# Kernel optimization log

Measured on AMD Instinct MI355X. Metric: run time of the kernel, lower is better.

## Reference

```python
import jax, jax.numpy as jnp
import numpy as np

# static config (mirrors params)
T, B, NA, NF = 48, 256, 23, 4
D = NA * NF          # y_dim = 92
XD = 2               # x_dim
H = 128              # rnn_dim
HD = 128             # h_dim
NL = 2               # n_layers
FS = 0.1
BURN = 12
IN_ENC = XD + D + H  # GRU input size = 222
A0, A1 = 12, 11      # agents 0..11 -> net0, 12..22 -> net1


def setup_inputs() -> dict:
    key = jax.random.key(0)
    ks = jax.random.split(key, 16)
    s = 0.05
    rn = lambda k, shape: jax.random.normal(k, shape, jnp.float32) * s
    return {
        "states": jax.random.normal(ks[0], (T + 1, 1, B, D), jnp.float32),
        # per-network (leading dim 2) GRU layer-0 and layer-1 weights (torch GRU layout: [r|z|n])
        "W_ih0": rn(ks[1], (2, 3 * H, IN_ENC)),
        "W_hh0": rn(ks[2], (2, 3 * H, H)),
        "b_ih0": rn(ks[3], (2, 3 * H)),
        "b_hh0": rn(ks[4], (2, 3 * H)),
        "W_ih1": rn(ks[5], (2, 3 * H, H)),
        "W_hh1": rn(ks[6], (2, 3 * H, H)),
        "b_ih1": rn(ks[7], (2, 3 * H)),
        "b_hh1": rn(ks[8], (2, 3 * H)),
        # decoder MLP (dropout is identity in eval) + mean head
        "W1": rn(ks[9], (2, HD, H)),
        "b1": rn(ks[10], (2, HD)),
        "W2": rn(ks[11], (2, HD, HD)),
        "b2": rn(ks[12], (2, HD)),
        "Wm": rn(ks[13], (2, XD, HD)),
        "bm": rn(ks[14], (2, XD)),
        "rollout": 0,
        "train": 0,
    }


def _gru_cell(x, h, Wih, Whh, bih, bhh):
    gi = x @ Wih.T + bih
    gh = h @ Whh.T + bhh
    r = jax.nn.sigmoid(gi[:, :H] + gh[:, :H])
    z = jax.nn.sigmoid(gi[:, H:2 * H] + gh[:, H:2 * H])
    n = jnp.tanh(gi[:, 2 * H:] + r * gh[:, 2 * H:])
    return (1.0 - z) * n + z * h


def _batch_error(a, b):
    # sum over batch of the euclidean norm over features
    return jnp.sum(jnp.sqrt(jnp.sum((a - b) ** 2, axis=1)))


def _group_step(h, y_t, y3, y3n, lo, hi, g, P):
    # h: [NL, A*B, H]; agents lo..hi-1 of network g, folded into the batch dim
    A = hi - lo
    vel = y3[:, lo:hi, 2:4].transpose(1, 0, 2).reshape(A * B, 2)
    pos = y3[:, lo:hi, 0:2].transpose(1, 0, 2).reshape(A * B, 2)
    vel_true = y3n[:, lo:hi, 2:4].transpose(1, 0, 2).reshape(A * B, 2)
    pos_true = y3n[:, lo:hi, 0:2].transpose(1, 0, 2).reshape(A * B, 2)
    y_rep = jnp.broadcast_to(y_t[None], (A, B, D)).reshape(A * B, D)
    h_last = h[-1]
    enc_in = jnp.concatenate([vel, y_rep, h_last], axis=1)  # [A*B, IN_ENC]
    # decoder uses the PRE-update hidden state
    d = jax.nn.relu(h_last @ P["W1"][g].T + P["b1"][g])
    d = jax.nn.relu(d @ P["W2"][g].T + P["b2"][g])
    dm = d @ P["Wm"][g].T + P["bm"][g]  # [A*B, XD]
    # 2-layer GRU step
    h0n = _gru_cell(enc_in, h[0], P["W_ih0"][g], P["W_hh0"][g], P["b_ih0"][g], P["b_hh0"][g])
    h1n = _gru_cell(h0n, h[1], P["W_ih1"][g], P["W_hh1"][g], P["b_ih1"][g], P["b_hh1"][g])
    h_new = jnp.stack([h0n, h1n])
    L = _batch_error(dm, vel_true)
    ep = _batch_error(pos + vel * FS, pos_true)
    ev = _batch_error(dm[:, :2], vel_true)
    return h_new, L, ep, ev


def _forward(states, P):
    y_seq = states[:T, 0]       # [T, B, D]
    y_next = states[1:T + 1, 0]  # [T, B, D]

    def step(carry, xs):
        h0, h1, L, ep, ev = carry
        y_t, y_t1, t = xs
        y3 = y_t.reshape(B, NA, NF)
        y3n = y_t1.reshape(B, NA, NF)
        h0n, L0, ep0, ev0 = _group_step(h0, y_t, y3, y3n, 0, A0, 0, P)
        h1n, L1, ep1, ev1 = _group_step(h1, y_t, y3, y3n, A0, NA, 1, P)
        m = (t >= BURN).astype(jnp.float32)
        return (h0n, h1n, L + L0 + L1, ep + m * (ep0 + ep1), ev + m * (ev0 + ev1)), None

    init = (jnp.zeros((NL, A0 * B, H), jnp.float32),
            jnp.zeros((NL, A1 * B, H), jnp.float32),
            jnp.zeros((), jnp.float32), jnp.zeros((), jnp.float32), jnp.zeros((), jnp.float32))
    (h0, h1, L, ep, ev), _ = jax.lax.scan(step, init, (y_seq, y_next, jnp.arange(T)))
    L_rec = L / (T * NA)
    e_pos = ep / ((T - BURN) * NA)
    e_vel = ev / ((T - BURN) * NA)
    return L_rec, e_pos, e_vel


def reference(states, W_ih0, W_hh0, b_ih0, b_hh0, W_ih1, W_hh1, b_ih1, b_hh1,
              W1, b1, W2, b2, Wm, bm, rollout, train):
    P = dict(W_ih0=W_ih0, W_hh0=W_hh0, b_ih0=b_ih0, b_hh0=b_hh0,
             W_ih1=W_ih1, W_hh1=W_hh1, b_ih1=b_ih1, b_hh1=b_hh1,
             W1=W1, b1=b1, W2=W2, b2=b2, Wm=Wm, bm=bm)
    return _forward(states, P)
```

## Files before the change

kernel.cpp:

```cpp
#include <hip/hip_runtime.h>
#include <hip/hip_bf16.h>


typedef unsigned short u16;
typedef unsigned int u32;
typedef unsigned char u8;
typedef long i64;
typedef __attribute__((ext_vector_type(4))) float f32x4;

#define MFMA_F8(acc, a, b) (acc) = __builtin_amdgcn_mfma_f32_16x16x32_fp8_fp8((i64)(a), (i64)(b), (acc), 0, 0, 0)

__device__ __forceinline__ void pin(i64& x) { asm volatile("" : "+v"(x)); }

__device__ __forceinline__ u8 f2e4(float v) {
  return (u8)(__builtin_amdgcn_cvt_pk_fp8_f32(v, 0.f, 0, false) & 0xff);
}
__device__ __forceinline__ u32 pk4(float a, float b, float c, float d) {
  u32 p = (u32)__builtin_amdgcn_cvt_pk_fp8_f32(a, b, 0, false);
  return (u32)__builtin_amdgcn_cvt_pk_fp8_f32(c, d, (int)p, true);
}
__device__ __forceinline__ float sigf(float x) {
  return __builtin_amdgcn_rcpf(1.f + __expf(-x));
}
__device__ __forceinline__ float tanh_fast(float x) {
  return 1.f - 2.f * __builtin_amdgcn_rcpf(1.f + __expf(2.f * x));
}

constexpr int E0 = 2 * 384 * 352;
constexpr int E1 = E0 + 2 * 384 * 256;
constexpr int E2 = E1 + 2 * 128 * 128;
constexpr int E3 = E2 + 2 * 128 * 128;
constexpr int E4 = E3 + 2 * 128 * 128;
constexpr int E5 = E4 + 2 * 128 * 128;
constexpr int NBIAS = 2048;
constexpr int TOTAL = E5 + NBIAS + 4;
constexpr int WB_BYTE_OFF = 16384;

__global__ void prep_kernel(const float* __restrict__ Wih0, const float* __restrict__ Whh0,
                            const float* __restrict__ bih0, const float* __restrict__ bhh0,
                            const float* __restrict__ Wih1, const float* __restrict__ Whh1,
                            const float* __restrict__ bih1, const float* __restrict__ bhh1,
                            const float* __restrict__ W1, const float* __restrict__ W2,
                            u8* __restrict__ wb, float* __restrict__ wsf) {
  for (int idx = blockIdx.x * blockDim.x + threadIdx.x; idx < TOTAL;
       idx += gridDim.x * blockDim.x) {
    if (idx < E0) {
      int g = idx / 135168;
      int r = idx - g * 135168;
      int j = r / 352;
      int k = r - j * 352;
      const float* wi = Wih0 + (g * 384 + j) * 222;
      float v;
      if (k < 94) v = wi[k];
      else if (k < 96) v = 0.f;
      else if (k < 224) v = wi[k - 2];
      else v = Whh0[(g * 384 + j) * 128 + (k - 224)];
      wb[idx] = f2e4(v);
    } else if (idx < E1) {
      int q = idx - E0;
      int g = q / 98304;
      int r = q - g * 98304;
      int j = r >> 8;
      int k = r & 255;
      float v = (k < 128) ? Wih1[(g * 384 + j) * 128 + k]
                          : Whh1[(g * 384 + j) * 128 + (k - 128)];
      wb[idx] = f2e4(v);
    } else if (idx < E2) {
      int q = idx - E1; int g = q >> 14; int r = q & 16383; int j = r >> 7; int k = r & 127;
      wb[idx] = f2e4(Whh0[(g * 384 + 256 + j) * 128 + k]);
    } else if (idx < E3) {
      int q = idx - E2; int g = q >> 14; int r = q & 16383; int j = r >> 7; int k = r & 127;
      wb[idx] = f2e4(Whh1[(g * 384 + 256 + j) * 128 + k]);
    } else if (idx < E4) {
      int q = idx - E3; int g = q >> 14; int r = q & 16383; int j = r >> 7; int k = r & 127;
      wb[idx] = f2e4(W1[(g * 128 + j) * 128 + k]);
    } else if (idx < E5) {
      int q = idx - E4; int g = q >> 14; int r = q & 16383; int j = r >> 7; int k = r & 127;
      wb[idx] = f2e4(W2[(g * 128 + j) * 128 + k]);
    } else if (idx < E5 + NBIAS) {
      int q = idx - E5;
      float v;
      if (q < 512)       { int g = q >> 8, j = q & 255;              v = bih0[g*384 + j] + bhh0[g*384 + j]; }
      else if (q < 768)  { int p = q - 512;  int g = p >> 7, j = p & 127; v = bih0[g*384 + 256 + j]; }
      else if (q < 1024) { int p = q - 768;  int g = p >> 7, j = p & 127; v = bhh0[g*384 + 256 + j]; }
      else if (q < 1536) { int p = q - 1024; int g = p >> 8, j = p & 255; v = bih1[g*384 + j] + bhh1[g*384 + j]; }
      else if (q < 1792) { int p = q - 1536; int g = p >> 7, j = p & 127; v = bih1[g*384 + 256 + j]; }
      else               { int p = q - 1792; int g = p >> 7, j = p & 127; v = bhh1[g*384 + 256 + j]; }
      wsf[4 + q] = v;
    } else {
      wsf[idx - (E5 + NBIAS)] = 0.f;
    }
  }
}

__global__ __launch_bounds__(512, 2) __attribute__((amdgpu_waves_per_eu(2, 2)))
void rnn_kernel(const float* __restrict__ states,
                const u8* __restrict__ wb,
                float* __restrict__ wsf,
                const float* __restrict__ b1g,
                const float* __restrict__ b2g,
                const float* __restrict__ Wmg,
                const float* __restrict__ bmg) {
  const int blk = blockIdx.x;
  const int g = (blk < 96) ? 0 : 1;
  const int r0 = (g == 0) ? (blk * 32) : ((blk - 96) * 32);
  const int aAg = (g == 0 ? 0 : 12) + (r0 >> 8);
  const int b0 = r0 & 255;

  const int tid = threadIdx.x;
  const int wid = tid >> 6;
  const int ln = tid & 63;
  const int j_in = ln & 15;
  const int kq = ln >> 4;
  const int c0 = wid * 16 + kq * 4;

  __shared__ __align__(16) u8 h0b[2][32 * 136];
  __shared__ __align__(16) u8 h1b[2][32 * 136];
  __shared__ __align__(16) u8 yb[2][32 * 104];
  __shared__ __align__(16) u8 d1b[32 * 136];
  __shared__ __align__(16) u8 d2b[32 * 136];
  __shared__ __align__(16) float bias[1536];
  __shared__ float dmv[48][32][2];
  __shared__ float red[8][3];

  const u8* W0   = wb + g * 135168;
  const u8* W1c  = wb + E0 + g * 98304;
  const u8* Wn0p = wb + E1 + g * 16384;
  const u8* Wn1p = wb + E2 + g * 16384;
  const u8* Wm1p = wb + E3 + g * 16384;
  const u8* Wm2p = wb + E4 + g * 16384;
  const int jh = wid * 16 + j_in;

  i64 w0r[11], w0z[11], w0n[7];
#pragma unroll
  for (int kt = 0; kt < 11; ++kt) {
    w0r[kt] = *(const i64*)(W0 + (jh)       * 352 + kt * 32 + kq * 8);
    w0z[kt] = *(const i64*)(W0 + (128 + jh) * 352 + kt * 32 + kq * 8);
    if (kt < 7) w0n[kt] = *(const i64*)(W0 + (256 + jh) * 352 + kt * 32 + kq * 8);
  }
  i64 w1r[8], w1z[8], w1n[4];
#pragma unroll
  for (int kt = 0; kt < 8; ++kt) {
    w1r[kt] = *(const i64*)(W1c + (jh)       * 256 + kt * 32 + kq * 8);
    w1z[kt] = *(const i64*)(W1c + (128 + jh) * 256 + kt * 32 + kq * 8);
    if (kt < 4) w1n[kt] = *(const i64*)(W1c + (256 + jh) * 256 + kt * 32 + kq * 8);
  }
  i64 wn0[4], wn1[4], wm1[4], wm2[4];
#pragma unroll
  for (int kt = 0; kt < 4; ++kt) {
    wn0[kt] = *(const i64*)(Wn0p + jh * 128 + kt * 32 + kq * 8);
    wn1[kt] = *(const i64*)(Wn1p + jh * 128 + kt * 32 + kq * 8);
    wm1[kt] = *(const i64*)(Wm1p + jh * 128 + kt * 32 + kq * 8);
    wm2[kt] = *(const i64*)(Wm2p + jh * 128 + kt * 32 + kq * 8);
  }
#pragma unroll
  for (int kt = 0; kt < 11; ++kt) { pin(w0r[kt]); pin(w0z[kt]); }
#pragma unroll
  for (int kt = 0; kt < 7; ++kt) pin(w0n[kt]);
#pragma unroll
  for (int kt = 0; kt < 8; ++kt) { pin(w1r[kt]); pin(w1z[kt]); }
#pragma unroll
  for (int kt = 0; kt < 4; ++kt) {
    pin(w1n[kt]); pin(wn0[kt]); pin(wn1[kt]); pin(wm1[kt]); pin(wm2[kt]);
  }

  for (int i = tid; i < 1536; i += 512) {
    float v;
    if (i < 256)       v = wsf[4 + g * 256 + i];
    else if (i < 384)  v = wsf[516 + g * 128 + (i - 256)];
    else if (i < 512)  v = wsf[772 + g * 128 + (i - 384)];
    else if (i < 768)  v = wsf[1028 + g * 256 + (i - 512)];
    else if (i < 896)  v = wsf[1540 + g * 128 + (i - 768)];
    else if (i < 1024) v = wsf[1796 + g * 128 + (i - 896)];
    else if (i < 1152) v = b1g[g * 128 + (i - 1024)];
    else if (i < 1280) v = b2g[g * 128 + (i - 1152)];
    else               v = Wmg[g * 256 + (i - 1280)];
    bias[i] = v;
  }
  for (int i = tid; i < 32 * 136; i += 512) { h0b[0][i] = 0; h1b[0][i] = 0; }
  for (int idx = tid; idx < 768; idx += 512) {
    int i = idx / 24, k4 = idx - i * 24;
    const float* srow = states + ((size_t)(b0 + i)) * 92;
    float v0, v1, v2, v3;
    if (k4 == 0) { v0 = srow[aAg*4+2]; v1 = srow[aAg*4+3]; v2 = srow[0]; v3 = srow[1]; }
    else {
      int kk = k4 * 4 - 2;
      v0 = srow[kk]; v1 = srow[kk+1];
      v2 = (kk+2 < 92) ? srow[kk+2] : 0.f;
      v3 = (kk+3 < 92) ? srow[kk+3] : 0.f;
    }
    *(u32*)(&yb[0][i * 104 + k4 * 4]) = pk4(v0, v1, v2, v3);
  }

  f32x4 hv0[2] = {{0,0,0,0},{0,0,0,0}};
  f32x4 hv1[2] = {{0,0,0,0},{0,0,0,0}};
  __syncthreads();

  for (int t = 0; t < 48; ++t) {
    const int cur = t & 1, nxt = cur ^ 1;
    const u8* h0c = h0b[cur]; u8* h0n = h0b[nxt];
    const u8* h1c = h1b[cur]; u8* h1n = h1b[nxt];
    const u8* ybc = yb[cur];  u8* ybn = yb[nxt];

    float yst[2][4];
#pragma unroll
    for (int q = 0; q < 2; ++q) {
      int idx = tid + q * 512;
      if (idx < 768) {
        int i = idx / 24, k4 = idx - i * 24;
        const float* srow = states + ((size_t)((t + 1) * 256 + b0 + i)) * 92;
        if (k4 == 0) { yst[q][0]=srow[aAg*4+2]; yst[q][1]=srow[aAg*4+3]; yst[q][2]=srow[0]; yst[q][3]=srow[1]; }
        else {
          int kk = k4 * 4 - 2;
          yst[q][0] = srow[kk]; yst[q][1] = srow[kk+1];
          yst[q][2] = (kk+2 < 92) ? srow[kk+2] : 0.f;
          yst[q][3] = (kk+3 < 92) ? srow[kk+3] : 0.f;
        }
      }
    }

    const u8* pH1a = h1c + j_in * 136 + kq * 8;
    const u8* pH1b = h1c + (16 + j_in) * 136 + kq * 8;
    const u8* pH0a = h0c + j_in * 136 + kq * 8;
    const u8* pH0b = h0c + (16 + j_in) * 136 + kq * 8;
    const u8* pYa  = ybc + j_in * 104 + kq * 8;
    const u8* pYb  = ybc + (16 + j_in) * 104 + kq * 8;

    {
      f32x4 m0 = {0,0,0,0}, m1 = {0,0,0,0};
#pragma unroll
      for (int kt = 0; kt < 4; ++kt) {
        i64 bb0 = *(const i64*)(pH1a + kt * 32);
        i64 bb1 = *(const i64*)(pH1b + kt * 32);
        MFMA_F8(m0, wm1[kt], bb0);
        MFMA_F8(m1, wm1[kt], bb1);
      }
      f32x4 b1v = *(const f32x4*)(bias + 1024 + c0);
      *(u32*)(d1b + j_in * 136 + c0) =
        pk4(fmaxf(m0[0]+b1v[0],0.f), fmaxf(m0[1]+b1v[1],0.f), fmaxf(m0[2]+b1v[2],0.f), fmaxf(m0[3]+b1v[3],0.f));
      *(u32*)(d1b + (16 + j_in) * 136 + c0) =
        pk4(fmaxf(m1[0]+b1v[0],0.f), fmaxf(m1[1]+b1v[1],0.f), fmaxf(m1[2]+b1v[2],0.f), fmaxf(m1[3]+b1v[3],0.f));
    }

    {
      f32x4 aR[2] = {{0,0,0,0},{0,0,0,0}};
      f32x4 aZ[2] = {{0,0,0,0},{0,0,0,0}};
      f32x4 aN[2] = {{0,0,0,0},{0,0,0,0}};
      f32x4 aG[2] = {{0,0,0,0},{0,0,0,0}};
#pragma unroll
      for (int kt = 0; kt < 11; ++kt) {
        i64 bb0, bb1;
        if (kt < 3)      { bb0 = *(const i64*)(pYa + kt * 32);        bb1 = *(const i64*)(pYb + kt * 32); }
        else if (kt < 7) { bb0 = *(const i64*)(pH1a + (kt - 3) * 32); bb1 = *(const i64*)(pH1b + (kt - 3) * 32); }
        else             { bb0 = *(const i64*)(pH0a + (kt - 7) * 32); bb1 = *(const i64*)(pH0b + (kt - 7) * 32); }
        MFMA_F8(aR[0], w0r[kt], bb0); MFMA_F8(aR[1], w0r[kt], bb1);
        MFMA_F8(aZ[0], w0z[kt], bb0); MFMA_F8(aZ[1], w0z[kt], bb1);
        if (kt < 7) { MFMA_F8(aN[0], w0n[kt], bb0); MFMA_F8(aN[1], w0n[kt], bb1); }
        else        { MFMA_F8(aG[0], wn0[kt - 7], bb0); MFMA_F8(aG[1], wn0[kt - 7], bb1); }
      }
      f32x4 brv = *(const f32x4*)(bias + c0);
      f32x4 bzv = *(const f32x4*)(bias + 128 + c0);
      f32x4 biv = *(const f32x4*)(bias + 256 + c0);
      f32x4 bhv = *(const f32x4*)(bias + 384 + c0);
#pragma unroll
      for (int nt = 0; nt < 2; ++nt)
#pragma unroll
        for (int i = 0; i < 4; ++i) {
          float rv = sigf(aR[nt][i] + brv[i]);
          float zv = sigf(aZ[nt][i] + bzv[i]);
          float nv = tanh_fast(aN[nt][i] + biv[i] + rv * (aG[nt][i] + bhv[i]));
          hv0[nt][i] = (1.f - zv) * nv + zv * hv0[nt][i];
        }
    }
    __syncthreads();

#pragma unroll
    for (int nt = 0; nt < 2; ++nt)
      *(u32*)(h0n + (nt * 16 + j_in) * 136 + c0) = pk4(hv0[nt][0], hv0[nt][1], hv0[nt][2], hv0[nt][3]);
    {
      f32x4 m0 = {0,0,0,0}, m1 = {0,0,0,0};
#pragma unroll
      for (int kt = 0; kt < 4; ++kt) {
        i64 bb0 = *(const i64*)(d1b + j_in * 136 + kt * 32 + kq * 8);
        i64 bb1 = *(const i64*)(d1b + (16 + j_in) * 136 + kt * 32 + kq * 8);
        MFMA_F8(m0, wm2[kt], bb0);
        MFMA_F8(m1, wm2[kt], bb1);
      }
      f32x4 b2v = *(const f32x4*)(bias + 1152 + c0);
      *(u32*)(d2b + j_in * 136 + c0) =
        pk4(fmaxf(m0[0]+b2v[0],0.f), fmaxf(m0[1]+b2v[1],0.f), fmaxf(m0[2]+b2v[2],0.f), fmaxf(m0[3]+b2v[3],0.f));
      *(u32*)(d2b + (16 + j_in) * 136 + c0) =
        pk4(fmaxf(m1[0]+b2v[0],0.f), fmaxf(m1[1]+b2v[1],0.f), fmaxf(m1[2]+b2v[2],0.f), fmaxf(m1[3]+b2v[3],0.f));
    }
    __syncthreads();

    {
      f32x4 aR[2] = {{0,0,0,0},{0,0,0,0}};
      f32x4 aZ[2] = {{0,0,0,0},{0,0,0,0}};
      f32x4 aN[2] = {{0,0,0,0},{0,0,0,0}};
      f32x4 aG[2] = {{0,0,0,0},{0,0,0,0}};
      const u8* pG0a = h0n + j_in * 136 + kq * 8;
      const u8* pG0b = h0n + (16 + j_in) * 136 + kq * 8;
#pragma unroll
      for (int kt = 0; kt < 8; ++kt) {
        i64 bb0, bb1;
        if (kt < 4) { bb0 = *(const i64*)(pG0a + kt * 32);        bb1 = *(const i64*)(pG0b + kt * 32); }
        else        { bb0 = *(const i64*)(pH1a + (kt - 4) * 32);  bb1 = *(const i64*)(pH1b + (kt - 4) * 32); }
        MFMA_F8(aR[0], w1r[kt], bb0); MFMA_F8(aR[1], w1r[kt], bb1);
        MFMA_F8(aZ[0], w1z[kt], bb0); MFMA_F8(aZ[1], w1z[kt], bb1);
        if (kt < 4) { MFMA_F8(aN[0], w1n[kt], bb0); MFMA_F8(aN[1], w1n[kt], bb1); }
        else        { MFMA_F8(aG[0], wn1[kt - 4], bb0); MFMA_F8(aG[1], wn1[kt - 4], bb1); }
      }
      {
        int row = tid >> 4, c = (tid >> 3) & 1, part = tid & 7;
        const u8* dp = d2b + row * 136 + part * 16;
        const float* wmr = bias + 1280 + c * 128 + part * 16;
        float s = 0.f;
#pragma unroll
        for (int q = 0; q < 4; ++q) {
          u32 w = *(const u32*)(dp + q * 4);
          s += wmr[q * 4 + 0] * __builtin_amdgcn_cvt_f32_fp8((int)w, 0);
          s += wmr[q * 4 + 1] * __builtin_amdgcn_cvt_f32_fp8((int)w, 1);
          s += wmr[q * 4 + 2] * __builtin_amdgcn_cvt_f32_fp8((int)w, 2);
          s += wmr[q * 4 + 3] * __builtin_amdgcn_cvt_f32_fp8((int)w, 3);
        }
        s += __shfl_xor(s, 1); s += __shfl_xor(s, 2); s += __shfl_xor(s, 4);
        if (part == 0) dmv[t][row][c] = s;
      }
      f32x4 brv = *(const f32x4*)(bias + 512 + c0);
      f32x4 bzv = *(const f32x4*)(bias + 640 + c0);
      f32x4 biv = *(const f32x4*)(bias + 768 + c0);
      f32x4 bhv = *(const f32x4*)(bias + 896 + c0);
#pragma unroll
      for (int nt = 0; nt < 2; ++nt)
#pragma unroll
        for (int i = 0; i < 4; ++i) {
          float rv = sigf(aR[nt][i] + brv[i]);
          float zv = sigf(aZ[nt][i] + bzv[i]);
          float nv = tanh_fast(aN[nt][i] + biv[i] + rv * (aG[nt][i] + bhv[i]));
          hv1[nt][i] = (1.f - zv) * nv + zv * hv1[nt][i];
        }
#pragma unroll
      for (int nt = 0; nt < 2; ++nt)
        *(u32*)(h1n + (nt * 16 + j_in) * 136 + c0) = pk4(hv1[nt][0], hv1[nt][1], hv1[nt][2], hv1[nt][3]);
    }
#pragma unroll
    for (int q = 0; q < 2; ++q) {
      int idx = tid + q * 512;
      if (idx < 768) {
        int i = idx / 24, k4 = idx - i * 24;
        *(u32*)(ybn + i * 104 + k4 * 4) = pk4(yst[q][0], yst[q][1], yst[q][2], yst[q][3]);
      }
    }
    __syncthreads();
  }

  float accL = 0.f, accEp = 0.f, accEv = 0.f;
  const float bm0 = bmg[g * 2], bm1 = bmg[g * 2 + 1];
  for (int idx = tid; idx < 1536; idx += 512) {
    int t = idx >> 5, row = idx & 31;
    const float* sr = states + ((size_t)(t * 256 + b0 + row)) * 92 + aAg * 4;
    const float* sn = sr + 256 * 92;
    float dx = dmv[t][row][0] + bm0 - sn[2];
    float dy = dmv[t][row][1] + bm1 - sn[3];
    float e = sqrtf(dx * dx + dy * dy);
    accL += e;
    if (t >= 12) {
      accEv += e;
      float ex = sr[0] + 0.1f * sr[2] - sn[0];
      float ey = sr[1] + 0.1f * sr[3] - sn[1];
      accEp += sqrtf(ex * ex + ey * ey);
    }
  }
#pragma unroll
  for (int k = 1; k < 64; k <<= 1) {
    accL  += __shfl_xor(accL, k);
    accEp += __shfl_xor(accEp, k);
    accEv += __shfl_xor(accEv, k);
  }
  if (ln == 0) { red[wid][0] = accL; red[wid][1] = accEp; red[wid][2] = accEv; }
  __syncthreads();
  if (tid < 3) {
    float s = 0.f;
    for (int i = 0; i < 8; ++i) s += red[i][tid];
    atomicAdd(&wsf[tid], s);
  }
}

__global__ void fin_kernel(const float* __restrict__ wacc, float* __restrict__ out) {
  if (threadIdx.x == 0 && blockIdx.x == 0) {
    out[0] = wacc[0] / 1104.f;
    out[1] = wacc[1] / 828.f;
    out[2] = wacc[2] / 828.f;
  }
}

extern "C" void kernel_launch(void* const* d_in, const int* in_sizes, int n_in,
                              void* d_out, int out_size, void* d_ws, size_t ws_size,
                              hipStream_t stream) {
  const float* states = (const float*)d_in[0];
  const float* Wih0 = (const float*)d_in[1];
  const float* Whh0 = (const float*)d_in[2];
  const float* bih0 = (const float*)d_in[3];
  const float* bhh0 = (const float*)d_in[4];
  const float* Wih1 = (const float*)d_in[5];
  const float* Whh1 = (const float*)d_in[6];
  const float* bih1 = (const float*)d_in[7];
  const float* bhh1 = (const float*)d_in[8];
  const float* W1   = (const float*)d_in[9];
  const float* b1   = (const float*)d_in[10];
  const float* W2   = (const float*)d_in[11];
  const float* b2   = (const float*)d_in[12];
  const float* Wm   = (const float*)d_in[13];
  const float* bm   = (const float*)d_in[14];

  float* wsf = (float*)d_ws;
  u8* wb = (u8*)d_ws + WB_BYTE_OFF;

  int prep_blocks = (TOTAL + 255) / 256;
  prep_kernel<<<prep_blocks, 256, 0, stream>>>(Wih0, Whh0, bih0, bhh0,
                                               Wih1, Whh1, bih1, bhh1,
                                               W1, W2, wb, wsf);
  rnn_kernel<<<184, 512, 0, stream>>>(states, wb, wsf, b1, b2, Wm, bm);
  fin_kernel<<<1, 64, 0, stream>>>(wsf, (float*)d_out);
}
```

Measured before the change: 321.8 us.

## Defer decoder mean head one step and drop a per-step barrier

The mean-head dot product for step t-1 now runs in the layer-0 phase of step t, reading d2b before the barrier. This lets one __syncthreads per timestep be removed, and the h0 store moves before that barrier. The loss is now accumulated per step by 32 threads instead of in a separate epilogue pass over a 48-step dmv buffer, which shrinks shared memory. Per-thread state-gather offsets are precomputed once so the loop no longer redoes the index divisions. The risk is correctness of the reordered d2b/d1b hazards, since the d2b write and the read from the previous step now depend on the remaining barriers.

```diff
diff --git a/kernel.cpp b/kernel.cpp
--- a/kernel.cpp
+++ b/kernel.cpp
@@ -113,6 +113,7 @@
   const int j_in = ln & 15;
   const int kq = ln >> 4;
   const int c0 = wid * 16 + kq * 4;
+  const int jh = wid * 16 + j_in;
 
   __shared__ __align__(16) u8 h0b[2][32 * 136];
   __shared__ __align__(16) u8 h1b[2][32 * 136];
@@ -120,8 +121,8 @@
   __shared__ __align__(16) u8 d1b[32 * 136];
   __shared__ __align__(16) u8 d2b[32 * 136];
   __shared__ __align__(16) float bias[1536];
-  __shared__ float dmv[48][32][2];
-  __shared__ float red[8][3];
+  __shared__ float dmv[32][2];
+  __shared__ float red[32][3];
 
   const u8* W0   = wb + g * 135168;
   const u8* W1c  = wb + E0 + g * 98304;
@@ -129,7 +130,6 @@
   const u8* Wn1p = wb + E2 + g * 16384;
   const u8* Wm1p = wb + E3 + g * 16384;
   const u8* Wm2p = wb + E4 + g * 16384;
-  const int jh = wid * 16 + j_in;
 
   i64 w0r[11], w0z[11], w0n[7];
 #pragma unroll
@@ -178,22 +178,37 @@
     bias[i] = v;
   }
   for (int i = tid; i < 32 * 136; i += 512) { h0b[0][i] = 0; h1b[0][i] = 0; }
-  for (int idx = tid; idx < 768; idx += 512) {
+
+  int sI[2], sK[2], sO0[2], sO1[2], sO2[2], sO3[2];
+  bool sZ2[2], sZ3[2], sV[2];
+#pragma unroll
+  for (int q = 0; q < 2; ++q) {
+    int idx = tid + q * 512;
+    sV[q] = (idx < 768);
     int i = idx / 24, k4 = idx - i * 24;
-    const float* srow = states + ((size_t)(b0 + i)) * 92;
-    float v0, v1, v2, v3;
-    if (k4 == 0) { v0 = srow[aAg*4+2]; v1 = srow[aAg*4+3]; v2 = srow[0]; v3 = srow[1]; }
+    sI[q] = i; sK[q] = k4;
+    if (k4 == 0) { sO0[q]=aAg*4+2; sO1[q]=aAg*4+3; sO2[q]=0; sO3[q]=1; sZ2[q]=false; sZ3[q]=false; }
     else {
       int kk = k4 * 4 - 2;
-      v0 = srow[kk]; v1 = srow[kk+1];
-      v2 = (kk+2 < 92) ? srow[kk+2] : 0.f;
-      v3 = (kk+3 < 92) ? srow[kk+3] : 0.f;
-    }
-    *(u32*)(&yb[0][i * 104 + k4 * 4]) = pk4(v0, v1, v2, v3);
-  }
-
+      sO0[q]=kk; sO1[q]=kk+1; sO2[q]=kk+2; sO3[q]=kk+3;
+      sZ2[q] = (kk+2 >= 92); sZ3[q] = (kk+3 >= 92);
+    }
+  }
+#pragma unroll
+  for (int q = 0; q < 2; ++q) {
+    if (sV[q]) {
+      const float* srow = states + ((size_t)(b0 + sI[q])) * 92;
+      float v0 = srow[sO0[q]], v1 = srow[sO1[q]];
+      float v2 = sZ2[q] ? 0.f : srow[sO2[q]];
+      float v3 = sZ3[q] ? 0.f : srow[sO3[q]];
+      *(u32*)(&yb[0][sI[q] * 104 + sK[q] * 4]) = pk4(v0, v1, v2, v3);
+    }
+  }
+
+  const float bm0 = bmg[g * 2], bm1 = bmg[g * 2 + 1];
   f32x4 hv0[2] = {{0,0,0,0},{0,0,0,0}};
   f32x4 hv1[2] = {{0,0,0,0},{0,0,0,0}};
+  float accL = 0.f, accEp = 0.f, accEv = 0.f;
   __syncthreads();
 
   for (int t = 0; t < 48; ++t) {
@@ -202,20 +217,14 @@
     const u8* h1c = h1b[cur]; u8* h1n = h1b[nxt];
     const u8* ybc = yb[cur];  u8* ybn = yb[nxt];
 
-    float yst[2][4];
+    float yv0[2], yv1[2], yv2[2], yv3[2];
 #pragma unroll
     for (int q = 0; q < 2; ++q) {
-      int idx = tid + q * 512;
-      if (idx < 768) {
-        int i = idx / 24, k4 = idx - i * 24;
-        const float* srow = states + ((size_t)((t + 1) * 256 + b0 + i)) * 92;
-        if (k4 == 0) { yst[q][0]=srow[aAg*4+2]; yst[q][1]=srow[aAg*4+3]; yst[q][2]=srow[0]; yst[q][3]=srow[1]; }
-        else {
-          int kk = k4 * 4 - 2;
-          yst[q][0] = srow[kk]; yst[q][1] = srow[kk+1];
-          yst[q][2] = (kk+2 < 92) ? srow[kk+2] : 0.f;
-          yst[q][3] = (kk+3 < 92) ? srow[kk+3] : 0.f;
-        }
+      if (sV[q]) {
+        const float* srow = states + ((size_t)((t + 1) * 256 + b0 + sI[q])) * 92;
+        yv0[q] = srow[sO0[q]]; yv1[q] = srow[sO1[q]];
+        yv2[q] = sZ2[q] ? 0.f : srow[sO2[q]];
+        yv3[q] = sZ3[q] ? 0.f : srow[sO3[q]];
       }
     }
 
@@ -271,12 +280,44 @@
           float nv = tanh_fast(aN[nt][i] + biv[i] + rv * (aG[nt][i] + bhv[i]));
           hv0[nt][i] = (1.f - zv) * nv + zv * hv0[nt][i];
         }
+#pragma unroll
+      for (int nt = 0; nt < 2; ++nt)
+        *(u32*)(h0n + (nt * 16 + j_in) * 136 + c0) = pk4(hv0[nt][0], hv0[nt][1], hv0[nt][2], hv0[nt][3]);
+    }
+
+    {
+      int row = tid >> 4, c = (tid >> 3) & 1, part = tid & 7;
+      const u8* dp = d2b + row * 136 + part * 16;
+      const float* wmr = bias + 1280 + c * 128 + part * 16;
+      float s = 0.f;
+#pragma unroll
+      for (int q = 0; q < 4; ++q) {
+        u32 w = *(const u32*)(dp + q * 4);
+        s += wmr[q * 4 + 0] * __builtin_amdgcn_cvt_f32_fp8((int)w, 0);
+        s += wmr[q * 4 + 1] * __builtin_amdgcn_cvt_f32_fp8((int)w, 1);
+        s += wmr[q * 4 + 2] * __builtin_amdgcn_cvt_f32_fp8((int)w, 2);
+        s += wmr[q * 4 + 3] * __builtin_amdgcn_cvt_f32_fp8((int)w, 3);
+      }
+      s += __shfl_xor(s, 1); s += __shfl_xor(s, 2); s += __shfl_xor(s, 4);
+      if (part == 0) dmv[row][c] = s;
     }
     __syncthreads();
 
-#pragma unroll
-    for (int nt = 0; nt < 2; ++nt)
-      *(u32*)(h0n + (nt * 16 + j_in) * 136 + c0) = pk4(hv0[nt][0], hv0[nt][1], hv0[nt][2], hv0[nt][3]);
+    if (t > 0 && tid < 32) {
+      const float* sr = states + ((size_t)((t - 1) * 256 + b0 + tid)) * 92 + aAg * 4;
+      const float* sn = sr + 256 * 92;
+      float dx = dmv[tid][0] + bm0 - sn[2];
+      float dy = dmv[tid][1] + bm1 - sn[3];
+      float e = sqrtf(dx * dx + dy * dy);
+      accL += e;
+      if (t - 1 >= 12) {
+        accEv += e;
+        float ex = sr[0] + 0.1f * sr[2] - sn[0];
+        float ey = sr[1] + 0.1f * sr[3] - sn[1];
+        accEp += sqrtf(ex * ex + ey * ey);
+      }
+    }
+
     {
       f32x4 m0 = {0,0,0,0}, m1 = {0,0,0,0};
 #pragma unroll
@@ -292,7 +333,6 @@
       *(u32*)(d2b + (16 + j_in) * 136 + c0) =
         pk4(fmaxf(m1[0]+b2v[0],0.f), fmaxf(m1[1]+b2v[1],0.f), fmaxf(m1[2]+b2v[2],0.f), fmaxf(m1[3]+b2v[3],0.f));
     }
-    __syncthreads();
 
     {
       f32x4 aR[2] = {{0,0,0,0},{0,0,0,0}};
@@ -311,22 +351,6 @@
         if (kt < 4) { MFMA_F8(aN[0], w1n[kt], bb0); MFMA_F8(aN[1], w1n[kt], bb1); }
         else        { MFMA_F8(aG[0], wn1[kt - 4], bb0); MFMA_F8(aG[1], wn1[kt - 4], bb1); }
       }
-      {
-        int row = tid >> 4, c = (tid >> 3) & 1, part = tid & 7;
-        const u8* dp = d2b + row * 136 + part * 16;
-        const float* wmr = bias + 1280 + c * 128 + part * 16;
-        float s = 0.f;
-#pragma unroll
-        for (int q = 0; q < 4; ++q) {
-          u32 w = *(const u32*)(dp + q * 4);
-          s += wmr[q * 4 + 0] * __builtin_amdgcn_cvt_f32_fp8((int)w, 0);
-          s += wmr[q * 4 + 1] * __builtin_amdgcn_cvt_f32_fp8((int)w, 1);
-          s += wmr[q * 4 + 2] * __builtin_amdgcn_cvt_f32_fp8((int)w, 2);
-          s += wmr[q * 4 + 3] * __builtin_amdgcn_cvt_f32_fp8((int)w, 3);
-        }
-        s += __shfl_xor(s, 1); s += __shfl_xor(s, 2); s += __shfl_xor(s, 4);
-        if (part == 0) dmv[t][row][c] = s;
-      }
       f32x4 brv = *(const f32x4*)(bias + 512 + c0);
       f32x4 bzv = *(const f32x4*)(bias + 640 + c0);
       f32x4 biv = *(const f32x4*)(bias + 768 + c0);
@@ -344,45 +368,50 @@
       for (int nt = 0; nt < 2; ++nt)
         *(u32*)(h1n + (nt * 16 + j_in) * 136 + c0) = pk4(hv1[nt][0], hv1[nt][1], hv1[nt][2], hv1[nt][3]);
     }
+
 #pragma unroll
     for (int q = 0; q < 2; ++q) {
-      int idx = tid + q * 512;
-      if (idx < 768) {
-        int i = idx / 24, k4 = idx - i * 24;
-        *(u32*)(ybn + i * 104 + k4 * 4) = pk4(yst[q][0], yst[q][1], yst[q][2], yst[q][3]);
+      if (sV[q]) {
+        *(u32*)(ybn + sI[q] * 104 + sK[q] * 4) = pk4(yv0[q], yv1[q], yv2[q], yv3[q]);
       }
     }
     __syncthreads();
   }
 
-  float accL = 0.f, accEp = 0.f, accEv = 0.f;
-  const float bm0 = bmg[g * 2], bm1 = bmg[g * 2 + 1];
-  for (int idx = tid; idx < 1536; idx += 512) {
-    int t = idx >> 5, row = idx & 31;
-    const float* sr = states + ((size_t)(t * 256 + b0 + row)) * 92 + aAg * 4;
+  {
+    int row = tid >> 4, c = (tid >> 3) & 1, part = tid & 7;
+    const u8* dp = d2b + row * 136 + part * 16;
+    const float* wmr = bias + 1280 + c * 128 + part * 16;
+    float s = 0.f;
+#pragma unroll
+    for (int q = 0; q < 4; ++q) {
+      u32 w = *(const u32*)(dp + q * 4);
+      s += wmr[q * 4 + 0] * __builtin_amdgcn_cvt_f32_fp8((int)w, 0);
+      s += wmr[q * 4 + 1] * __builtin_amdgcn_cvt_f32_fp8((int)w, 1);
+      s += wmr[q * 4 + 2] * __builtin_amdgcn_cvt_f32_fp8((int)w, 2);
+      s += wmr[q * 4 + 3] * __builtin_amdgcn_cvt_f32_fp8((int)w, 3);
+    }
+    s += __shfl_xor(s, 1); s += __shfl_xor(s, 2); s += __shfl_xor(s, 4);
+    if (part == 0) dmv[row][c] = s;
+  }
+  __syncthreads();
+  if (tid < 32) {
+    const float* sr = states + ((size_t)(47 * 256 + b0 + tid)) * 92 + aAg * 4;
     const float* sn = sr + 256 * 92;
-    float dx = dmv[t][row][0] + bm0 - sn[2];
-    float dy = dmv[t][row][1] + bm1 - sn[3];
+    float dx = dmv[tid][0] + bm0 - sn[2];
+    float dy = dmv[tid][1] + bm1 - sn[3];
     float e = sqrtf(dx * dx + dy * dy);
     accL += e;
-    if (t >= 12) {
-      accEv += e;
-      float ex = sr[0] + 0.1f * sr[2] - sn[0];
-      float ey = sr[1] + 0.1f * sr[3] - sn[1];
-      accEp += sqrtf(ex * ex + ey * ey);
-    }
-  }
-#pragma unroll
-  for (int k = 1; k < 64; k <<= 1) {
-    accL  += __shfl_xor(accL, k);
-    accEp += __shfl_xor(accEp, k);
-    accEv += __shfl_xor(accEv, k);
-  }
-  if (ln == 0) { red[wid][0] = accL; red[wid][1] = accEp; red[wid][2] = accEv; }
+    accEv += e;
+    float ex = sr[0] + 0.1f * sr[2] - sn[0];
+    float ey = sr[1] + 0.1f * sr[3] - sn[1];
+    accEp += sqrtf(ex * ex + ey * ey);
+    red[tid][0] = accL; red[tid][1] = accEp; red[tid][2] = accEv;
+  }
   __syncthreads();
   if (tid < 3) {
     float s = 0.f;
-    for (int i = 0; i < 8; ++i) s += red[i][tid];
+    for (int i = 0; i < 32; ++i) s += red[i][tid];
     atomicAdd(&wsf[tid], s);
   }
 }
```

Measured after the change: 335.5 us. 4.2% more time.

## Move decoder MLP out of recurrent loop into separate parallel kernel

Applied to the files above, without the earlier changes.

The decoder MLP and loss computation leave the sequential RNN loop. The RNN kernel now writes each step's layer-1 hidden state to global memory as fp8, and a new mlp_kernel with 736 blocks processes those states in parallel over time chunks. Per-agent input weights with the velocity/position fold and fp8-converted states are precomputed in prep, so y loads become direct register fetches prefetched one step ahead, and one __syncthreads per step is removed. The cost is a larger prep pass (about 2.4M extra elements to convert), roughly 37MB of extra global traffic for the stored hidden states, and an extra kernel launch.

```diff
diff --git a/kernel.cpp b/kernel.cpp
--- a/kernel.cpp
+++ b/kernel.cpp
@@ -36,13 +36,23 @@
 constexpr int TOTAL = E5 + NBIAS + 4;
 constexpr int WB_BYTE_OFF = 16384;
 
-__global__ void prep_kernel(const float* __restrict__ Wih0, const float* __restrict__ Whh0,
+constexpr int WYA_REL = E5;
+constexpr int YBG_REL = WYA_REL + 23 * 384 * 96;
+constexpr int H1G_REL = YBG_REL + 48 * 256 * 96;
+
+constexpr int NA1 = TOTAL;
+constexpr int NA2 = NA1 + 23 * 384 * 96;
+constexpr int NA3 = NA2 + 48 * 256 * 96;
+constexpr int NA4 = NA3 + 184 * 4096;
+
+__global__ void prep_kernel(const float* __restrict__ states,
+                            const float* __restrict__ Wih0, const float* __restrict__ Whh0,
                             const float* __restrict__ bih0, const float* __restrict__ bhh0,
                             const float* __restrict__ Wih1, const float* __restrict__ Whh1,
                             const float* __restrict__ bih1, const float* __restrict__ bhh1,
                             const float* __restrict__ W1, const float* __restrict__ W2,
                             u8* __restrict__ wb, float* __restrict__ wsf) {
-  for (int idx = blockIdx.x * blockDim.x + threadIdx.x; idx < TOTAL;
+  for (int idx = blockIdx.x * blockDim.x + threadIdx.x; idx < NA4;
        idx += gridDim.x * blockDim.x) {
     if (idx < E0) {
       int g = idx / 135168;
@@ -87,20 +97,36 @@
       else if (q < 1792) { int p = q - 1536; int g = p >> 7, j = p & 127; v = bih1[g*384 + 256 + j]; }
       else               { int p = q - 1792; int g = p >> 7, j = p & 127; v = bhh1[g*384 + 256 + j]; }
       wsf[4 + q] = v;
+    } else if (idx < TOTAL) {
+      wsf[idx - (E5 + NBIAS)] = 0.f;
+    } else if (idx < NA2) {
+      int q = idx - NA1;
+      int a = q / 36864;
+      int r = q - a * 36864;
+      int j = r / 96;
+      int k = r - j * 96;
+      const float* wi = Wih0 + (((a >= 12) ? 1 : 0) * 384 + j) * 222;
+      float v = (k < 92) ? wi[2 + k] : 0.f;
+      if (k == a * 4 + 2) v += wi[0];
+      if (k == a * 4 + 3) v += wi[1];
+      wb[WYA_REL + q] = f2e4(v);
+    } else if (idx < NA3) {
+      int q = idx - NA2;
+      int t = q / 24576;
+      int r = q - t * 24576;
+      int row = r / 96;
+      int k = r - row * 96;
+      float v = (k < 92) ? states[((size_t)t * 256 + row) * 92 + k] : 0.f;
+      wb[YBG_REL + q] = f2e4(v);
     } else {
-      wsf[idx - (E5 + NBIAS)] = 0.f;
+      wb[H1G_REL + (idx - NA3)] = 0;
     }
   }
 }
 
 __global__ __launch_bounds__(512, 2) __attribute__((amdgpu_waves_per_eu(2, 2)))
-void rnn_kernel(const float* __restrict__ states,
-                const u8* __restrict__ wb,
-                float* __restrict__ wsf,
-                const float* __restrict__ b1g,
-                const float* __restrict__ b2g,
-                const float* __restrict__ Wmg,
-                const float* __restrict__ bmg) {
+void rnn_kernel(const u8* __restrict__ wb, const float* __restrict__ wsf,
+                u8* __restrict__ h1g_base) {
   const int blk = blockIdx.x;
   const int g = (blk < 96) ? 0 : 1;
   const int r0 = (g == 0) ? (blk * 32) : ((blk - 96) * 32);
@@ -113,27 +139,29 @@
   const int j_in = ln & 15;
   const int kq = ln >> 4;
   const int c0 = wid * 16 + kq * 4;
+  const int jh = wid * 16 + j_in;
 
   __shared__ __align__(16) u8 h0b[2][32 * 136];
   __shared__ __align__(16) u8 h1b[2][32 * 136];
-  __shared__ __align__(16) u8 yb[2][32 * 104];
-  __shared__ __align__(16) u8 d1b[32 * 136];
-  __shared__ __align__(16) u8 d2b[32 * 136];
-  __shared__ __align__(16) float bias[1536];
-  __shared__ float dmv[48][32][2];
-  __shared__ float red[8][3];
+  __shared__ __align__(16) float bias[1024];
 
   const u8* W0   = wb + g * 135168;
   const u8* W1c  = wb + E0 + g * 98304;
   const u8* Wn0p = wb + E1 + g * 16384;
   const u8* Wn1p = wb + E2 + g * 16384;
-  const u8* Wm1p = wb + E3 + g * 16384;
-  const u8* Wm2p = wb + E4 + g * 16384;
-  const int jh = wid * 16 + j_in;
+  const u8* WYA  = wb + WYA_REL + aAg * 36864;
+  const u8* YBG  = wb + YBG_REL;
+  u8* H1G = h1g_base + blk * 200704;
 
   i64 w0r[11], w0z[11], w0n[7];
 #pragma unroll
-  for (int kt = 0; kt < 11; ++kt) {
+  for (int kt = 0; kt < 3; ++kt) {
+    w0r[kt] = *(const i64*)(WYA + (jh)       * 96 + kt * 32 + kq * 8);
+    w0z[kt] = *(const i64*)(WYA + (128 + jh) * 96 + kt * 32 + kq * 8);
+    w0n[kt] = *(const i64*)(WYA + (256 + jh) * 96 + kt * 32 + kq * 8);
+  }
+#pragma unroll
+  for (int kt = 3; kt < 11; ++kt) {
     w0r[kt] = *(const i64*)(W0 + (jh)       * 352 + kt * 32 + kq * 8);
     w0z[kt] = *(const i64*)(W0 + (128 + jh) * 352 + kt * 32 + kq * 8);
     if (kt < 7) w0n[kt] = *(const i64*)(W0 + (256 + jh) * 352 + kt * 32 + kq * 8);
@@ -145,13 +173,11 @@
     w1z[kt] = *(const i64*)(W1c + (128 + jh) * 256 + kt * 32 + kq * 8);
     if (kt < 4) w1n[kt] = *(const i64*)(W1c + (256 + jh) * 256 + kt * 32 + kq * 8);
   }
-  i64 wn0[4], wn1[4], wm1[4], wm2[4];
+  i64 wn0[4], wn1[4];
 #pragma unroll
   for (int kt = 0; kt < 4; ++kt) {
     wn0[kt] = *(const i64*)(Wn0p + jh * 128 + kt * 32 + kq * 8);
     wn1[kt] = *(const i64*)(Wn1p + jh * 128 + kt * 32 + kq * 8);
-    wm1[kt] = *(const i64*)(Wm1p + jh * 128 + kt * 32 + kq * 8);
-    wm2[kt] = *(const i64*)(Wm2p + jh * 128 + kt * 32 + kq * 8);
   }
 #pragma unroll
   for (int kt = 0; kt < 11; ++kt) { pin(w0r[kt]); pin(w0z[kt]); }
@@ -160,36 +186,28 @@
 #pragma unroll
   for (int kt = 0; kt < 8; ++kt) { pin(w1r[kt]); pin(w1z[kt]); }
 #pragma unroll
-  for (int kt = 0; kt < 4; ++kt) {
-    pin(w1n[kt]); pin(wn0[kt]); pin(wn1[kt]); pin(wm1[kt]); pin(wm2[kt]);
-  }
-
-  for (int i = tid; i < 1536; i += 512) {
+  for (int kt = 0; kt < 4; ++kt) { pin(w1n[kt]); pin(wn0[kt]); pin(wn1[kt]); }
+
+  for (int i = tid; i < 1024; i += 512) {
     float v;
     if (i < 256)       v = wsf[4 + g * 256 + i];
     else if (i < 384)  v = wsf[516 + g * 128 + (i - 256)];
     else if (i < 512)  v = wsf[772 + g * 128 + (i - 384)];
     else if (i < 768)  v = wsf[1028 + g * 256 + (i - 512)];
     else if (i < 896)  v = wsf[1540 + g * 128 + (i - 768)];
-    else if (i < 1024) v = wsf[1796 + g * 128 + (i - 896)];
-    else if (i < 1152) v = b1g[g * 128 + (i - 1024)];
-    else if (i < 1280) v = b2g[g * 128 + (i - 1152)];
-    else               v = Wmg[g * 256 + (i - 1280)];
+    else               v = wsf[1796 + g * 128 + (i - 896)];
     bias[i] = v;
   }
   for (int i = tid; i < 32 * 136; i += 512) { h0b[0][i] = 0; h1b[0][i] = 0; }
-  for (int idx = tid; idx < 768; idx += 512) {
-    int i = idx / 24, k4 = idx - i * 24;
-    const float* srow = states + ((size_t)(b0 + i)) * 92;
-    float v0, v1, v2, v3;
-    if (k4 == 0) { v0 = srow[aAg*4+2]; v1 = srow[aAg*4+3]; v2 = srow[0]; v3 = srow[1]; }
-    else {
-      int kk = k4 * 4 - 2;
-      v0 = srow[kk]; v1 = srow[kk+1];
-      v2 = (kk+2 < 92) ? srow[kk+2] : 0.f;
-      v3 = (kk+3 < 92) ? srow[kk+3] : 0.f;
-    }
-    *(u32*)(&yb[0][i * 104 + k4 * 4]) = pk4(v0, v1, v2, v3);
+
+  const u8* yA = YBG + (b0 + j_in) * 96 + kq * 8;
+  const u8* yB = YBG + (b0 + 16 + j_in) * 96 + kq * 8;
+
+  i64 yf[3][2];
+#pragma unroll
+  for (int kt = 0; kt < 3; ++kt) {
+    yf[kt][0] = *(const i64*)(yA + kt * 32);
+    yf[kt][1] = *(const i64*)(yB + kt * 32);
   }
 
   f32x4 hv0[2] = {{0,0,0,0},{0,0,0,0}};
@@ -200,46 +218,25 @@
     const int cur = t & 1, nxt = cur ^ 1;
     const u8* h0c = h0b[cur]; u8* h0n = h0b[nxt];
     const u8* h1c = h1b[cur]; u8* h1n = h1b[nxt];
-    const u8* ybc = yb[cur];  u8* ybn = yb[nxt];
-
-    float yst[2][4];
-#pragma unroll
-    for (int q = 0; q < 2; ++q) {
-      int idx = tid + q * 512;
-      if (idx < 768) {
-        int i = idx / 24, k4 = idx - i * 24;
-        const float* srow = states + ((size_t)((t + 1) * 256 + b0 + i)) * 92;
-        if (k4 == 0) { yst[q][0]=srow[aAg*4+2]; yst[q][1]=srow[aAg*4+3]; yst[q][2]=srow[0]; yst[q][3]=srow[1]; }
-        else {
-          int kk = k4 * 4 - 2;
-          yst[q][0] = srow[kk]; yst[q][1] = srow[kk+1];
-          yst[q][2] = (kk+2 < 92) ? srow[kk+2] : 0.f;
-          yst[q][3] = (kk+3 < 92) ? srow[kk+3] : 0.f;
-        }
-      }
+
+    const int tp = (t < 47) ? (t + 1) : 47;
+    i64 yn[3][2];
+#pragma unroll
+    for (int kt = 0; kt < 3; ++kt) {
+      yn[kt][0] = *(const i64*)(yA + tp * 24576 + kt * 32);
+      yn[kt][1] = *(const i64*)(yB + tp * 24576 + kt * 32);
     }
 
     const u8* pH1a = h1c + j_in * 136 + kq * 8;
     const u8* pH1b = h1c + (16 + j_in) * 136 + kq * 8;
     const u8* pH0a = h0c + j_in * 136 + kq * 8;
     const u8* pH0b = h0c + (16 + j_in) * 136 + kq * 8;
-    const u8* pYa  = ybc + j_in * 104 + kq * 8;
-    const u8* pYb  = ybc + (16 + j_in) * 104 + kq * 8;
-
-    {
-      f32x4 m0 = {0,0,0,0}, m1 = {0,0,0,0};
-#pragma unroll
-      for (int kt = 0; kt < 4; ++kt) {
-        i64 bb0 = *(const i64*)(pH1a + kt * 32);
-        i64 bb1 = *(const i64*)(pH1b + kt * 32);
-        MFMA_F8(m0, wm1[kt], bb0);
-        MFMA_F8(m1, wm1[kt], bb1);
-      }
-      f32x4 b1v = *(const f32x4*)(bias + 1024 + c0);
-      *(u32*)(d1b + j_in * 136 + c0) =
-        pk4(fmaxf(m0[0]+b1v[0],0.f), fmaxf(m0[1]+b1v[1],0.f), fmaxf(m0[2]+b1v[2],0.f), fmaxf(m0[3]+b1v[3],0.f));
-      *(u32*)(d1b + (16 + j_in) * 136 + c0) =
-        pk4(fmaxf(m1[0]+b1v[0],0.f), fmaxf(m1[1]+b1v[1],0.f), fmaxf(m1[2]+b1v[2],0.f), fmaxf(m1[3]+b1v[3],0.f));
+
+    i64 fh1[4][2];
+#pragma unroll
+    for (int kt = 0; kt < 4; ++kt) {
+      fh1[kt][0] = *(const i64*)(pH1a + kt * 32);
+      fh1[kt][1] = *(const i64*)(pH1b + kt * 32);
     }
 
     {
@@ -250,9 +247,10 @@
 #pragma unroll
       for (int kt = 0; kt < 11; ++kt) {
         i64 bb0, bb1;
-        if (kt < 3)      { bb0 = *(const i64*)(pYa + kt * 32);        bb1 = *(const i64*)(pYb + kt * 32); }
-        else if (kt < 7) { bb0 = *(const i64*)(pH1a + (kt - 3) * 32); bb1 = *(const i64*)(pH1b + (kt - 3) * 32); }
-        else             { bb0 = *(const i64*)(pH0a + (kt - 7) * 32); bb1 = *(const i64*)(pH0b + (kt - 7) * 32); }
+        if (kt < 3)      { bb0 = yf[kt][0];      bb1 = yf[kt][1]; }
+        else if (kt < 7) { bb0 = fh1[kt - 3][0]; bb1 = fh1[kt - 3][1]; }
+        else             { bb0 = *(const i64*)(pH0a + (kt - 7) * 32);
+                           bb1 = *(const i64*)(pH0b + (kt - 7) * 32); }
         MFMA_F8(aR[0], w0r[kt], bb0); MFMA_F8(aR[1], w0r[kt], bb1);
         MFMA_F8(aZ[0], w0z[kt], bb0); MFMA_F8(aZ[1], w0z[kt], bb1);
         if (kt < 7) { MFMA_F8(aN[0], w0n[kt], bb0); MFMA_F8(aN[1], w0n[kt], bb1); }
@@ -271,26 +269,9 @@
           float nv = tanh_fast(aN[nt][i] + biv[i] + rv * (aG[nt][i] + bhv[i]));
           hv0[nt][i] = (1.f - zv) * nv + zv * hv0[nt][i];
         }
-    }
-    __syncthreads();
-
-#pragma unroll
-    for (int nt = 0; nt < 2; ++nt)
-      *(u32*)(h0n + (nt * 16 + j_in) * 136 + c0) = pk4(hv0[nt][0], hv0[nt][1], hv0[nt][2], hv0[nt][3]);
-    {
-      f32x4 m0 = {0,0,0,0}, m1 = {0,0,0,0};
-#pragma unroll
-      for (int kt = 0; kt < 4; ++kt) {
-        i64 bb0 = *(const i64*)(d1b + j_in * 136 + kt * 32 + kq * 8);
-        i64 bb1 = *(const i64*)(d1b + (16 + j_in) * 136 + kt * 32 + kq * 8);
-        MFMA_F8(m0, wm2[kt], bb0);
-        MFMA_F8(m1, wm2[kt], bb1);
-      }
-      f32x4 b2v = *(const f32x4*)(bias + 1152 + c0);
-      *(u32*)(d2b + j_in * 136 + c0) =
-        pk4(fmaxf(m0[0]+b2v[0],0.f), fmaxf(m0[1]+b2v[1],0.f), fmaxf(m0[2]+b2v[2],0.f), fmaxf(m0[3]+b2v[3],0.f));
-      *(u32*)(d2b + (16 + j_in) * 136 + c0) =
-        pk4(fmaxf(m1[0]+b2v[0],0.f), fmaxf(m1[1]+b2v[1],0.f), fmaxf(m1[2]+b2v[2],0.f), fmaxf(m1[3]+b2v[3],0.f));
+#pragma unroll
+      for (int nt = 0; nt < 2; ++nt)
+        *(u32*)(h0n + (nt * 16 + j_in) * 136 + c0) = pk4(hv0[nt][0], hv0[nt][1], hv0[nt][2], hv0[nt][3]);
     }
     __syncthreads();
 
@@ -304,28 +285,12 @@
 #pragma unroll
       for (int kt = 0; kt < 8; ++kt) {
         i64 bb0, bb1;
-        if (kt < 4) { bb0 = *(const i64*)(pG0a + kt * 32);        bb1 = *(const i64*)(pG0b + kt * 32); }
-        else        { bb0 = *(const i64*)(pH1a + (kt - 4) * 32);  bb1 = *(const i64*)(pH1b + (kt - 4) * 32); }
+        if (kt < 4) { bb0 = *(const i64*)(pG0a + kt * 32); bb1 = *(const i64*)(pG0b + kt * 32); }
+        else        { bb0 = fh1[kt - 4][0];                bb1 = fh1[kt - 4][1]; }
         MFMA_F8(aR[0], w1r[kt], bb0); MFMA_F8(aR[1], w1r[kt], bb1);
         MFMA_F8(aZ[0], w1z[kt], bb0); MFMA_F8(aZ[1], w1z[kt], bb1);
         if (kt < 4) { MFMA_F8(aN[0], w1n[kt], bb0); MFMA_F8(aN[1], w1n[kt], bb1); }
         else        { MFMA_F8(aG[0], wn1[kt - 4], bb0); MFMA_F8(aG[1], wn1[kt - 4], bb1); }
-      }
-      {
-        int row = tid >> 4, c = (tid >> 3) & 1, part = tid & 7;
-        const u8* dp = d2b + row * 136 + part * 16;
-        const float* wmr = bias + 1280 + c * 128 + part * 16;
-        float s = 0.f;
-#pragma unroll
-        for (int q = 0; q < 4; ++q) {
-          u32 w = *(const u32*)(dp + q * 4);
-          s += wmr[q * 4 + 0] * __builtin_amdgcn_cvt_f32_fp8((int)w, 0);
-          s += wmr[q * 4 + 1] * __builtin_amdgcn_cvt_f32_fp8((int)w, 1);
-          s += wmr[q * 4 + 2] * __builtin_amdgcn_cvt_f32_fp8((int)w, 2);
-          s += wmr[q * 4 + 3] * __builtin_amdgcn_cvt_f32_fp8((int)w, 3);
-        }
-        s += __shfl_xor(s, 1); s += __shfl_xor(s, 2); s += __shfl_xor(s, 4);
-        if (part == 0) dmv[t][row][c] = s;
       }
       f32x4 brv = *(const f32x4*)(bias + 512 + c0);
       f32x4 bzv = *(const f32x4*)(bias + 640 + c0);
@@ -341,49 +306,148 @@
           hv1[nt][i] = (1.f - zv) * nv + zv * hv1[nt][i];
         }
 #pragma unroll
-      for (int nt = 0; nt < 2; ++nt)
-        *(u32*)(h1n + (nt * 16 + j_in) * 136 + c0) = pk4(hv1[nt][0], hv1[nt][1], hv1[nt][2], hv1[nt][3]);
-    }
-#pragma unroll
-    for (int q = 0; q < 2; ++q) {
-      int idx = tid + q * 512;
-      if (idx < 768) {
-        int i = idx / 24, k4 = idx - i * 24;
-        *(u32*)(ybn + i * 104 + k4 * 4) = pk4(yst[q][0], yst[q][1], yst[q][2], yst[q][3]);
-      }
-    }
+      for (int nt = 0; nt < 2; ++nt) {
+        u32 p = pk4(hv1[nt][0], hv1[nt][1], hv1[nt][2], hv1[nt][3]);
+        *(u32*)(h1n + (nt * 16 + j_in) * 136 + c0) = p;
+        *(u32*)(H1G + (t + 1) * 4096 + (nt * 16 + j_in) * 128 + c0) = p;
+      }
+    }
+#pragma unroll
+    for (int kt = 0; kt < 3; ++kt) { yf[kt][0] = yn[kt][0]; yf[kt][1] = yn[kt][1]; }
     __syncthreads();
   }
-
+}
+
+__global__ __launch_bounds__(512)
+void mlp_kernel(const float* __restrict__ states,
+                const u8* __restrict__ wb,
+                float* __restrict__ wsf,
+                const float* __restrict__ b1g,
+                const float* __restrict__ b2g,
+                const float* __restrict__ Wmg,
+                const float* __restrict__ bmg) {
+  const int bi = blockIdx.x;
+  const int blkRow = bi >> 2;
+  const int chunk = bi & 3;
+  const int g = (blkRow < 96) ? 0 : 1;
+  const int r0 = (g == 0) ? (blkRow * 32) : ((blkRow - 96) * 32);
+  const int aAg = (g == 0 ? 0 : 12) + (r0 >> 8);
+  const int b0 = r0 & 255;
+
+  const int tid = threadIdx.x;
+  const int ln = tid & 63;
+  const int wid = tid >> 6;
+  const int j_in = ln & 15;
+  const int kq = ln >> 4;
+  const int c0 = wid * 16 + kq * 4;
+  const int jh = wid * 16 + j_in;
+
+  __shared__ __align__(16) u8 d1b[32 * 136];
+  __shared__ __align__(16) u8 d2b[32 * 136];
+  __shared__ __align__(16) float biasm[512];
+
+  const u8* Wm1p = wb + E3 + g * 16384;
+  const u8* Wm2p = wb + E4 + g * 16384;
+  const u8* H1Gm = wb + H1G_REL + blkRow * 200704;
+
+  i64 wm1[4], wm2[4];
+#pragma unroll
+  for (int kt = 0; kt < 4; ++kt) {
+    wm1[kt] = *(const i64*)(Wm1p + jh * 128 + kt * 32 + kq * 8);
+    wm2[kt] = *(const i64*)(Wm2p + jh * 128 + kt * 32 + kq * 8);
+  }
+  for (int i = tid; i < 512; i += 512) {
+    float v;
+    if (i < 128)      v = b1g[g * 128 + i];
+    else if (i < 256) v = b2g[g * 128 + (i - 128)];
+    else              v = Wmg[g * 256 + (i - 256)];
+    biasm[i] = v;
+  }
+  const float bm0 = bmg[g * 2], bm1 = bmg[g * 2 + 1];
   float accL = 0.f, accEp = 0.f, accEv = 0.f;
-  const float bm0 = bmg[g * 2], bm1 = bmg[g * 2 + 1];
-  for (int idx = tid; idx < 1536; idx += 512) {
-    int t = idx >> 5, row = idx & 31;
-    const float* sr = states + ((size_t)(t * 256 + b0 + row)) * 92 + aAg * 4;
-    const float* sn = sr + 256 * 92;
-    float dx = dmv[t][row][0] + bm0 - sn[2];
-    float dy = dmv[t][row][1] + bm1 - sn[3];
-    float e = sqrtf(dx * dx + dy * dy);
-    accL += e;
-    if (t >= 12) {
-      accEv += e;
-      float ex = sr[0] + 0.1f * sr[2] - sn[0];
-      float ey = sr[1] + 0.1f * sr[3] - sn[1];
-      accEp += sqrtf(ex * ex + ey * ey);
-    }
-  }
-#pragma unroll
-  for (int k = 1; k < 64; k <<= 1) {
-    accL  += __shfl_xor(accL, k);
-    accEp += __shfl_xor(accEp, k);
-    accEv += __shfl_xor(accEv, k);
-  }
-  if (ln == 0) { red[wid][0] = accL; red[wid][1] = accEp; red[wid][2] = accEv; }
   __syncthreads();
-  if (tid < 3) {
-    float s = 0.f;
-    for (int i = 0; i < 8; ++i) s += red[i][tid];
-    atomicAdd(&wsf[tid], s);
+
+  for (int ti = 0; ti < 12; ++ti) {
+    const int t = chunk * 12 + ti;
+    const u8* hb = H1Gm + t * 4096;
+
+    i64 fh[4][2];
+#pragma unroll
+    for (int kt = 0; kt < 4; ++kt) {
+      fh[kt][0] = *(const i64*)(hb + j_in * 128 + kt * 32 + kq * 8);
+      fh[kt][1] = *(const i64*)(hb + (16 + j_in) * 128 + kt * 32 + kq * 8);
+    }
+    {
+      f32x4 m0 = {0,0,0,0}, m1 = {0,0,0,0};
+#pragma unroll
+      for (int kt = 0; kt < 4; ++kt) {
+        MFMA_F8(m0, wm1[kt], fh[kt][0]);
+        MFMA_F8(m1, wm1[kt], fh[kt][1]);
+      }
+      f32x4 b1v = *(const f32x4*)(biasm + c0);
+      *(u32*)(d1b + j_in * 136 + c0) =
+        pk4(fmaxf(m0[0]+b1v[0],0.f), fmaxf(m0[1]+b1v[1],0.f), fmaxf(m0[2]+b1v[2],0.f), fmaxf(m0[3]+b1v[3],0.f));
+      *(u32*)(d1b + (16 + j_in) * 136 + c0) =
+        pk4(fmaxf(m1[0]+b1v[0],0.f), fmaxf(m1[1]+b1v[1],0.f), fmaxf(m1[2]+b1v[2],0.f), fmaxf(m1[3]+b1v[3],0.f));
+    }
+    __syncthreads();
+
+    {
+      f32x4 m0 = {0,0,0,0}, m1 = {0,0,0,0};
+#pragma unroll
+      for (int kt = 0; kt < 4; ++kt) {
+        i64 bb0 = *(const i64*)(d1b + j_in * 136 + kt * 32 + kq * 8);
+        i64 bb1 = *(const i64*)(d1b + (16 + j_in) * 136 + kt * 32 + kq * 8);
+        MFMA_F8(m0, wm2[kt], bb0);
+        MFMA_F8(m1, wm2[kt], bb1);
+      }
+      f32x4 b2v = *(const f32x4*)(biasm + 128 + c0);
+      *(u32*)(d2b + j_in * 136 + c0) =
+        pk4(fmaxf(m0[0]+b2v[0],0.f), fmaxf(m0[1]+b2v[1],0.f), fmaxf(m0[2]+b2v[2],0.f), fmaxf(m0[3]+b2v[3],0.f));
+      *(u32*)(d2b + (16 + j_in) * 136 + c0) =
+        pk4(fmaxf(m1[0]+b2v[0],0.f), fmaxf(m1[1]+b2v[1],0.f), fmaxf(m1[2]+b2v[2],0.f), fmaxf(m1[3]+b2v[3],0.f));
+    }
+    __syncthreads();
+
+    {
+      int row = tid >> 4, c = (tid >> 3) & 1, part = tid & 7;
+      const u8* dp = d2b + row * 136 + part * 16;
+      const float* wmr = biasm + 256 + c * 128 + part * 16;
+      float s = 0.f;
+#pragma unroll
+      for (int q = 0; q < 4; ++q) {
+        u32 w = *(const u32*)(dp + q * 4);
+        s += wmr[q * 4 + 0] * __builtin_amdgcn_cvt_f32_fp8((int)w, 0);
+        s += wmr[q * 4 + 1] * __builtin_amdgcn_cvt_f32_fp8((int)w, 1);
+        s += wmr[q * 4 + 2] * __builtin_amdgcn_cvt_f32_fp8((int)w, 2);
+        s += wmr[q * 4 + 3] * __builtin_amdgcn_cvt_f32_fp8((int)w, 3);
+      }
+      s += __shfl_xor(s, 1); s += __shfl_xor(s, 2); s += __shfl_xor(s, 4);
+      float so = __shfl_xor(s, 8);
+      if ((tid & 15) == 0) {
+        const float* sr = states + ((size_t)(t * 256 + b0 + row)) * 92 + aAg * 4;
+        const float* sn = sr + 256 * 92;
+        float dx = s + bm0 - sn[2];
+        float dy = so + bm1 - sn[3];
+        float e = sqrtf(dx * dx + dy * dy);
+        accL += e;
+        if (t >= 12) {
+          accEv += e;
+          float ex = sr[0] + 0.1f * sr[2] - sn[0];
+          float ey = sr[1] + 0.1f * sr[3] - sn[1];
+          accEp += sqrtf(ex * ex + ey * ey);
+        }
+      }
+    }
+  }
+
+  accL  += __shfl_xor(accL, 16);  accL  += __shfl_xor(accL, 32);
+  accEp += __shfl_xor(accEp, 16); accEp += __shfl_xor(accEp, 32);
+  accEv += __shfl_xor(accEv, 16); accEv += __shfl_xor(accEv, 32);
+  if (ln == 0) {
+    atomicAdd(&wsf[0], accL);
+    atomicAdd(&wsf[1], accEp);
+    atomicAdd(&wsf[2], accEv);
   }
 }
 
@@ -417,10 +481,11 @@
   float* wsf = (float*)d_ws;
   u8* wb = (u8*)d_ws + WB_BYTE_OFF;
 
-  int prep_blocks = (TOTAL + 255) / 256;
-  prep_kernel<<<prep_blocks, 256, 0, stream>>>(Wih0, Whh0, bih0, bhh0,
+  int prep_blocks = (NA4 + 255) / 256;
+  prep_kernel<<<prep_blocks, 256, 0, stream>>>(states, Wih0, Whh0, bih0, bhh0,
                                                Wih1, Whh1, bih1, bhh1,
                                                W1, W2, wb, wsf);
-  rnn_kernel<<<184, 512, 0, stream>>>(states, wb, wsf, b1, b2, Wm, bm);
+  rnn_kernel<<<184, 512, 0, stream>>>(wb, wsf, wb + H1G_REL);
+  mlp_kernel<<<736, 512, 0, stream>>>(states, wb, wsf, b1, b2, Wm, bm);
   fin_kernel<<<1, 64, 0, stream>>>(wsf, (float*)d_out);
 }
```

Result: slower. 547.9 us (+70.2%).
